# Optimization experiments

Measured on AMD Instinct MI355X. Metric: run time of the kernel, lower is better.

The kernel has to match this reference:

```python
import jax, jax.numpy as jnp
import numpy as np

EPS = 1e-5
N_LAYER = 2            # Mamba2 blocks per direction
D_STATE = 16
HEADDIM = 32
D_INNER = 256          # expand * d_model
NHEADS = D_INNER // HEADDIM
CONV_DIM = D_INNER + 2 * D_STATE
D_CONV = 4


def rmsnorm(x, w):
    return x * jax.lax.rsqrt(jnp.mean(x * x, axis=-1, keepdims=True) + EPS) * w


def causal_dwconv(x, w, b):
    # x: [B, L, C]; w: [C, K]; depthwise causal conv along L (torch conv1d groups=C, pad K-1, slice :L)
    out = jax.lax.conv_general_dilated(
        x.transpose(0, 2, 1), w[:, None, :], (1,), [(w.shape[1] - 1, 0)],
        dimension_numbers=('NCH', 'OIH', 'NCH'), feature_group_count=w.shape[0])
    return (out + b[:, None]).transpose(0, 2, 1)


def ssm_scan(dA, dtx, Bm, Cm):
    # dA:[B,L,H]  dtx:[B,L,H,P]  Bm,Cm:[B,L,N]  ->  y:[B,L,H,P]
    Bsz, L, H, P = dtx.shape
    N = Bm.shape[-1]
    h0 = jnp.zeros((Bsz, H, P, N), dtx.dtype)

    def step(h, ins):
        dA_t, dtx_t, B_t, C_t = ins
        h = h * dA_t[:, :, None, None] + jnp.einsum('bhp,bn->bhpn', dtx_t, B_t)
        return h, jnp.einsum('bhpn,bn->bhp', h, C_t)

    _, ys = jax.lax.scan(step, h0, (dA.transpose(1, 0, 2), dtx.transpose(1, 0, 2, 3),
                                    Bm.transpose(1, 0, 2), Cm.transpose(1, 0, 2)))
    return ys.transpose(1, 0, 2, 3)


def mamba2_block(h, in_w, cw, cb, dtb, a_log, d_skip, nw, ow):
    Bsz, L, _ = h.shape
    zxbcdt = jnp.einsum('bld,ed->ble', h, in_w)  # [B,L, 2*d_inner + 2*N + H]
    z = zxbcdt[..., :D_INNER]
    xBC = zxbcdt[..., D_INNER:D_INNER + CONV_DIM]
    dt = jax.nn.softplus(zxbcdt[..., D_INNER + CONV_DIM:] + dtb)  # [B,L,H]
    xBC = jax.nn.silu(causal_dwconv(xBC, cw, cb))
    xs = xBC[..., :D_INNER].reshape(Bsz, L, NHEADS, HEADDIM)
    Bm = xBC[..., D_INNER:D_INNER + D_STATE]
    Cm = xBC[..., D_INNER + D_STATE:]
    dA = jnp.exp(dt * (-jnp.exp(a_log)))                           # [B,L,H]
    y = ssm_scan(dA, dt[..., None] * xs, Bm, Cm) + d_skip[None, None, :, None] * xs
    y = rmsnorm(y.reshape(Bsz, L, D_INNER) * jax.nn.silu(z), nw)   # gated RMSNorm
    return jnp.einsum('ble,de->bld', y, ow)


def reference(x, buffer, fc_in_w, fc_in_b, blk_norm_w, in_proj_w, conv_w, conv_b,
              dt_bias, A_log, D, mixer_norm_w, out_proj_w, norm_f_w,
              fc_out_w, fc_out_b, out_lin_w, out_lin_b):
    n_state_buffer = buffer.shape[2]
    buf = jnp.concatenate([buffer, x[:, :, None]], axis=2)[:, :, -n_state_buffer:]
    h = jnp.einsum('bcl,dc->bld', buf, fc_in_w) + fc_in_b  # [B,L,d_model]

    def run_dir(hh, dir_idx):
        for l in range(N_LAYER):
            i = dir_idx * N_LAYER + l
            hh = hh + mamba2_block(rmsnorm(hh, blk_norm_w[i]), in_proj_w[i],
                                   conv_w[i], conv_b[i], dt_bias[i], A_log[i],
                                   D[i], mixer_norm_w[i], out_proj_w[i])
        return rmsnorm(hh, norm_f_w[dir_idx])

    hs = run_dir(h, 0) + jnp.flip(run_dir(jnp.flip(h, 1), 1), 1)
    y = jnp.einsum('bld,od->blo', hs, fc_out_w) + fc_out_b        # [B,L,cout]
    y = jnp.einsum('blo,kl->bok', y, out_lin_w)[..., 0] + out_lin_b[0]  # [B,cout]
    return y, buf


def setup_inputs():
    key = jax.random.key(0)
    ks = jax.random.split(key, 10)
    B, CIN, COUT, L, DM, NB = 1024, 96, 12, 32, 128, 4
    f = jnp.float32
    return {
        'x': jax.random.normal(ks[0], (B, CIN), f),
        'buffer': jax.random.normal(ks[1], (B, CIN, L), f),
        'fc_in_w': jax.random.normal(ks[2], (DM, CIN), f) * 0.05,
        'fc_in_b': jnp.zeros((DM,), f),
        'blk_norm_w': jnp.ones((NB, DM), f),
        'in_proj_w': jax.random.normal(ks[3], (NB, 2 * D_INNER + 2 * D_STATE + NHEADS, DM), f) * 0.05,
        'conv_w': jax.random.normal(ks[4], (NB, CONV_DIM, D_CONV), f) * 0.2,
        'conv_b': jnp.zeros((NB, CONV_DIM), f),
        'dt_bias': jax.random.normal(ks[5], (NB, NHEADS), f) * 0.1,
        'A_log': jnp.log(jax.random.uniform(ks[6], (NB, NHEADS), f, 1.0, 16.0)),
        'D': jnp.ones((NB, NHEADS), f),
        'mixer_norm_w': jnp.ones((NB, D_INNER), f),
        'out_proj_w': jax.random.normal(ks[7], (NB, DM, D_INNER), f) * 0.05,
        'norm_f_w': jnp.ones((2, DM), f),
        'fc_out_w': jax.random.normal(ks[8], (COUT, DM), f) * 0.05,
        'fc_out_b': jnp.zeros((COUT,), f),
        'out_lin_w': jax.random.normal(ks[9], (1, L), f) * 0.1,
        'out_lin_b': jnp.zeros((1,), f),
    }
```

## Files before the change

kernel.cpp:

```cpp
#include <hip/hip_runtime.h>
#include <hip/hip_bf16.h>
#include <math.h>

#define B_SZ   1024
#define CIN    96
#define COUT   12
#define LSEQ   32
#define DM     128
#define D_IN   256
#define D_ST   16
#define NH     8
#define HD     32
#define CONVD  288
#define EPROJ  552
#define EPSV   1e-5f

#define THREADS 512

typedef unsigned short ushort_t;
typedef unsigned int uint_t;
typedef __attribute__((ext_vector_type(8))) short short8;
typedef __attribute__((ext_vector_type(4))) float f32x4;

#define NIP (4*35*4*512)
#define NOP (4*8*8*512)
#define NFC (8*3*512)
__device__ ushort_t g_wip[NIP];
__device__ ushort_t g_wop[NOP];
__device__ ushort_t g_wfc[NFC];

__device__ __forceinline__ uint_t cvt2bf(float lo, float hi) {
    uint_t r;
    asm("v_cvt_pk_bf16_f32 %0, %1, %2" : "=v"(r) : "v"(lo), "v"(hi));
    return r;
}
__device__ __forceinline__ ushort_t f2bf(float f) {
    return (ushort_t)cvt2bf(f, f);
}
__device__ __forceinline__ float bf2f(ushort_t u) {
    return __uint_as_float((uint_t)u << 16);
}
__device__ __forceinline__ float siluf(float v) { return v / (1.f + __expf(-v)); }
__device__ __forceinline__ float softplusf_(float v) {
    return (v > 20.f) ? v : log1pf(__expf(v));
}

__device__ __forceinline__ ushort_t f2bf_sw(float f) {
    uint_t u = __float_as_uint(f);
    u += 0x7FFFu + ((u >> 16) & 1u);
    return (ushort_t)(u >> 16);
}

__global__ void prep_weights(const float* __restrict__ in_proj_w,
                             const float* __restrict__ out_proj_w,
                             const float* __restrict__ fc_in_w) {
    int idx = blockIdx.x * 256 + threadIdx.x;
    if (idx < NIP) {
        int f = idx >> 9, r = idx & 511;
        int l = r >> 3, j = r & 7;
        int li = f / 140, rem = f - li * 140;
        int nt = rem >> 2, kc = rem & 3;
        int e = nt * 16 + (l & 15);
        int d = kc * 32 + ((l >> 4) << 3) + j;
        float v = (e < EPROJ) ? in_proj_w[((size_t)li * EPROJ + e) * DM + d] : 0.f;
        g_wip[idx] = f2bf_sw(v);
    } else if (idx < NIP + NOP) {
        int i2 = idx - NIP;
        int f = i2 >> 9, r = i2 & 511;
        int l = r >> 3, j = r & 7;
        int li = f >> 6, rem = f & 63;
        int nt = rem >> 3, kc = rem & 7;
        int d = nt * 16 + (l & 15);
        int e = kc * 32 + ((l >> 4) << 3) + j;
        g_wop[i2] = f2bf_sw(out_proj_w[((size_t)li * DM + d) * D_IN + e]);
    } else if (idx < NIP + NOP + NFC) {
        int i2 = idx - NIP - NOP;
        int f = i2 >> 9, r = i2 & 511;
        int l = r >> 3, j = r & 7;
        int nt = f / 3, kc = f - nt * 3;
        int d = nt * 16 + (l & 15);
        int c = kc * 32 + ((l >> 4) << 3) + j;
        g_wfc[i2] = f2bf_sw(fc_in_w[d * CIN + c]);
    }
}

__global__ void init_out(const float* __restrict__ fc_out_b,
                         const float* __restrict__ out_lin_w,
                         const float* __restrict__ out_lin_b,
                         float* __restrict__ out_y) {
    int i = blockIdx.x * 256 + threadIdx.x;
    if (i >= B_SZ * COUT) return;
    int o = i % COUT;
    float s = 0.f;
#pragma unroll
    for (int t = 0; t < LSEQ; ++t) s += out_lin_w[t];
    out_y[i] = fc_out_b[o] * s + out_lin_b[0];
}

#define OFF_HH   0
#define OFF_BUFB 4224
#define OFF_HNB  6272
#define OFF_ZYB  8320
#define OFF_XB   12416
#define OFF_BCF  16512
#define OFF_DTA  17664
#define SMEM_WORDS 18176
#define SMEM_BYTES (SMEM_WORDS * 4)

__global__ __launch_bounds__(THREADS, 4)
void mamba_fused(const float* __restrict__ x,
                 const float* __restrict__ buffer,
                 const float* __restrict__ fc_in_b,
                 const float* __restrict__ blk_norm_w,
                 const float* __restrict__ conv_w,
                 const float* __restrict__ conv_b,
                 const float* __restrict__ dt_bias,
                 const float* __restrict__ A_log,
                 const float* __restrict__ D_skip,
                 const float* __restrict__ mixer_norm_w,
                 const float* __restrict__ norm_f_w,
                 const float* __restrict__ fc_out_w,
                 const float* __restrict__ out_lin_w,
                 float* __restrict__ out_y,
                 float* __restrict__ out_buf)
{
    const int b   = blockIdx.x >> 1;
    const int dir = blockIdx.x & 1;
    const int tid = threadIdx.x;

    extern __shared__ float sm[];
    float*    s_hh  = sm + OFF_HH;
    ushort_t* s_bufb= (ushort_t*)(sm + OFF_BUFB);
    ushort_t* s_hnb = (ushort_t*)(sm + OFF_HNB);
    ushort_t* s_zyb = (ushort_t*)(sm + OFF_ZYB);
    ushort_t* s_xb  = (ushort_t*)(sm + OFF_XB);
    float*    s_bcf = sm + OFF_BCF;
    float*    s_dtA = sm + OFF_DTA;

    const int wid  = tid >> 6;
    const int lane = tid & 63;
    const int quad = lane >> 4;

    {
        const float* bufp = buffer + (size_t)b * (CIN * LSEQ);
        const float* xp   = x + (size_t)b * CIN;
        float* obp        = out_buf + (size_t)b * (CIN * LSEQ);
        for (int i = tid; i < CIN * LSEQ; i += THREADS) {
            int c = i >> 5, l2 = i & 31;
            float v = (l2 < 31) ? bufp[i + 1] : xp[c];
            if (dir == 0) obp[i] = v;
            s_bufb[(l2 * 128 + c) ^ ((l2 & 7) << 3)] = f2bf(v);
        }
    }
    __syncthreads();

    {
        int mt = wid >> 2, row = mt * 16 + (lane & 15);
        const short8* ab = (const short8*)s_bufb;
        const ushort_t* wb = g_wfc + lane * 8;
#pragma unroll
        for (int pass = 0; pass < 2; ++pass) {
            int nt = (wid & 3) + pass * 4;
            f32x4 acc = {0.f, 0.f, 0.f, 0.f};
#pragma unroll
            for (int kc = 0; kc < 3; ++kc) {
                short8 av = ab[(row * 16 + kc * 4 + quad) ^ (row & 7)];
                short8 bv = *(const short8*)(wb + (nt * 3 + kc) * 512);
                acc = __builtin_amdgcn_mfma_f32_16x16x32_bf16(av, bv, acc, 0, 0, 0);
            }
            int d = nt * 16 + (lane & 15);
            float bias = fc_in_b[d];
#pragma unroll
            for (int r = 0; r < 4; ++r) {
                int t = mt * 16 + quad * 4 + r;
                int tt = dir ? (31 - t) : t;
                s_hh[tt * 132 + d] = acc[r] + bias;
            }
        }
    }
    __syncthreads();

    for (int lyr = 0; lyr < 2; ++lyr) {
        const int li = dir * 2 + lyr;

        {
            int t = tid >> 4, sl = tid & 15;
            const float* row = s_hh + t * 132;
            float v[8]; float ss = 0.f;
#pragma unroll
            for (int j = 0; j < 8; ++j) { v[j] = row[sl * 8 + j]; ss += v[j] * v[j]; }
            ss += __shfl_xor(ss, 1); ss += __shfl_xor(ss, 2);
            ss += __shfl_xor(ss, 4); ss += __shfl_xor(ss, 8);
            float scale = rsqrtf(ss * (1.f / DM) + EPSV);
            const float* nw = blk_norm_w + li * DM;
            uint_t w[4];
#pragma unroll
            for (int p = 0; p < 4; ++p) {
                int d0 = sl * 8 + p * 2;
                w[p] = cvt2bf(v[p * 2] * scale * nw[d0],
                              v[p * 2 + 1] * scale * nw[d0 + 1]);
            }
            uint4 q = make_uint4(w[0], w[1], w[2], w[3]);
            ((uint4*)s_hnb)[(t * 16 + sl) ^ (t & 7)] = q;
        }
        __syncthreads();

        {
            int mt = wid >> 2, row = mt * 16 + (lane & 15);
            const short8* ab = (const short8*)s_hnb;
            short8 a[4];
#pragma unroll
            for (int kc = 0; kc < 4; ++kc)
                a[kc] = ab[(row * 16 + kc * 4 + quad) ^ (row & 7)];

            const ushort_t* wbase = g_wip + (size_t)li * (35 * 4 * 512) + lane * 8;
            for (int nt = wid & 3; nt < 35; nt += 4) {
                f32x4 acc = {0.f, 0.f, 0.f, 0.f};
#pragma unroll
                for (int kc = 0; kc < 4; ++kc) {
                    short8 bv = *(const short8*)(wbase + (nt * 4 + kc) * 512);
                    acc = __builtin_amdgcn_mfma_f32_16x16x32_bf16(a[kc], bv, acc, 0, 0, 0);
                }
                int e = nt * 16 + (lane & 15);
#pragma unroll
                for (int r = 0; r < 4; ++r) {
                    int t = mt * 16 + quad * 4 + r;
                    float v = acc[r];
                    if (e < D_IN) {
                        s_zyb[(t * 256 + e) ^ ((t & 7) << 3)] = f2bf(siluf(v));
                    } else if (e < 512) {
                        s_xb[t * 256 + (e - D_IN)] = f2bf(v);
                    } else if (e < 544) {
                        s_bcf[t * 36 + (e - 512)] = v;
                    } else if (e < EPROJ) {
                        int hd2 = e - 544;
                        float dtv = softplusf_(v + dt_bias[li * NH + hd2]);
                        float aneg = -__expf(A_log[li * NH + hd2]);
                        s_dtA[t * 16 + hd2 * 2]     = dtv;
                        s_dtA[t * 16 + hd2 * 2 + 1] = __expf(dtv * aneg);
                    }
                }
            }
        }
        __syncthreads();

        if (tid < CONVD) {
            const int c = tid;
            const float4 wv = *(const float4*)(conv_w + ((size_t)li * CONVD + c) * 4);
            const float bias = conv_b[li * CONVD + c];
            float w0 = 0.f, w1 = 0.f, w2 = 0.f;
            if (c < D_IN) {
#pragma unroll
                for (int t = 0; t < 32; ++t) {
                    float cur = bf2f(s_xb[t * 256 + c]);
                    float acc = bias + w0 * wv.x + w1 * wv.y + w2 * wv.z + cur * wv.w;
                    s_xb[t * 256 + c] = f2bf(siluf(acc));
                    w0 = w1; w1 = w2; w2 = cur;
                }
            } else {
                const int ch = c - D_IN;
#pragma unroll
                for (int t = 0; t < 32; ++t) {
                    float cur = s_bcf[t * 36 + ch];
                    float acc = bias + w0 * wv.x + w1 * wv.y + w2 * wv.z + cur * wv.w;
                    s_bcf[t * 36 + ch] = siluf(acc);
                    w0 = w1; w1 = w2; w2 = cur;
                }
            }
        }
        __syncthreads();

        if (tid < 256) {
            int hd = tid >> 5, p = tid & 31;
            float dsk = D_skip[li * NH + hd];
            float st[16];
#pragma unroll
            for (int n = 0; n < 16; ++n) st[n] = 0.f;
#pragma unroll
            for (int t = 0; t < 32; ++t) {
                const float2 da = *(const float2*)(s_dtA + t * 16 + hd * 2);
                float dtv = da.x, dAv = da.y;
                float xsv = bf2f(s_xb[t * 256 + hd * HD + p]);
                float dtx = dtv * xsv;
                const f32x4* Bp = (const f32x4*)(s_bcf + t * 36);
                const f32x4* Cp = (const f32x4*)(s_bcf + t * 36 + 16);
                float acc0 = 0.f, acc1 = 0.f, acc2 = 0.f, acc3 = 0.f;
#pragma unroll
                for (int q = 0; q < 4; ++q) {
                    f32x4 Bv = Bp[q], Cv = Cp[q];
                    float* s4 = st + q * 4;
                    s4[0] = s4[0] * dAv + dtx * Bv.x;  acc0 += s4[0] * Cv.x;
                    s4[1] = s4[1] * dAv + dtx * Bv.y;  acc1 += s4[1] * Cv.y;
                    s4[2] = s4[2] * dAv + dtx * Bv.z;  acc2 += s4[2] * Cv.z;
                    s4[3] = s4[3] * dAv + dtx * Bv.w;  acc3 += s4[3] * Cv.w;
                }
                float y = (acc0 + acc1) + (acc2 + acc3) + dsk * xsv;
                s_xb[t * 256 + hd * HD + p] = f2bf(y);
            }
        }
        __syncthreads();

        {
            int t = tid >> 4, sl = tid & 15;
            float g[16]; float ss = 0.f;
#pragma unroll
            for (int j = 0; j < 16; ++j) {
                int e = j * 16 + sl;
                float yv = bf2f(s_xb[t * 256 + e]);
                float zv = bf2f(s_zyb[(t * 256 + e) ^ ((t & 7) << 3)]);
                float gv = yv * zv;
                g[j] = gv; ss += gv * gv;
            }
            ss += __shfl_xor(ss, 1); ss += __shfl_xor(ss, 2);
            ss += __shfl_xor(ss, 4); ss += __shfl_xor(ss, 8);
            float scale = rsqrtf(ss * (1.f / D_IN) + EPSV);
            const float* mw = mixer_norm_w + li * D_IN;
#pragma unroll
            for (int j = 0; j < 16; ++j) {
                int e = j * 16 + sl;
                s_zyb[(t * 256 + e) ^ ((t & 7) << 3)] = f2bf(g[j] * scale * mw[e]);
            }
        }
        __syncthreads();

        {
            int mt = wid >> 2, row = mt * 16 + (lane & 15);
            const short8* yb = (const short8*)s_zyb;
            const ushort_t* wb = g_wop + (size_t)li * (8 * 8 * 512) + lane * 8;
#pragma unroll
            for (int pass = 0; pass < 2; ++pass) {
                int nt = (wid & 3) + pass * 4;
                f32x4 acc = {0.f, 0.f, 0.f, 0.f};
#pragma unroll
                for (int kh = 0; kh < 2; ++kh) {
                    short8 a4[4];
#pragma unroll
                    for (int j = 0; j < 4; ++j)
                        a4[j] = yb[(row * 32 + (kh * 4 + j) * 4 + quad) ^ (row & 7)];
#pragma unroll
                    for (int j = 0; j < 4; ++j) {
                        short8 bv = *(const short8*)(wb + (nt * 8 + kh * 4 + j) * 512);
                        acc = __builtin_amdgcn_mfma_f32_16x16x32_bf16(a4[j], bv, acc, 0, 0, 0);
                    }
                }
                int d = nt * 16 + (lane & 15);
#pragma unroll
                for (int r = 0; r < 4; ++r)
                    s_hh[(mt * 16 + quad * 4 + r) * 132 + d] += acc[r];
            }
        }
        __syncthreads();
    }

    {
        int t = tid >> 4, sl = tid & 15;
        float* row = s_hh + t * 132;
        float v[8]; float ss = 0.f;
#pragma unroll
        for (int j = 0; j < 8; ++j) { v[j] = row[sl * 8 + j]; ss += v[j] * v[j]; }
        ss += __shfl_xor(ss, 1); ss += __shfl_xor(ss, 2);
        ss += __shfl_xor(ss, 4); ss += __shfl_xor(ss, 8);
        float scale = rsqrtf(ss * (1.f / DM) + EPSV);
        const float* nw = norm_f_w + dir * DM;
#pragma unroll
        for (int j = 0; j < 8; ++j) {
            int d = sl * 8 + j;
            row[d] = v[j] * scale * nw[d];
        }
    }
    __syncthreads();

    if (tid < COUT * LSEQ) {
        int o = tid >> 5, t = tid & 31;
        int t_out = dir ? (31 - t) : t;
        const float* wrow = fc_out_w + o * DM;
        const float* hrow = s_hh + t * 132;
        float acc = 0.f;
#pragma unroll
        for (int d = 0; d < DM; d += 4) {
            float4 wv = *(const float4*)(wrow + d);
            float4 hv = *(const float4*)(hrow + d);
            acc += hv.x * wv.x + hv.y * wv.y + hv.z * wv.z + hv.w * wv.w;
        }
        float part = acc * out_lin_w[t_out];
        part += __shfl_xor(part, 1);  part += __shfl_xor(part, 2);
        part += __shfl_xor(part, 4);  part += __shfl_xor(part, 8);
        part += __shfl_xor(part, 16);
        if (t == 0) atomicAdd(&out_y[b * COUT + o], part);
    }
}

extern "C" void kernel_launch(void* const* d_in, const int* in_sizes, int n_in,
                              void* d_out, int out_size, void* d_ws, size_t ws_size,
                              hipStream_t stream) {
    const float* x            = (const float*)d_in[0];
    const float* buffer      = (const float*)d_in[1];
    const float* fc_in_w     = (const float*)d_in[2];
    const float* fc_in_b     = (const float*)d_in[3];
    const float* blk_norm_w  = (const float*)d_in[4];
    const float* in_proj_w   = (const float*)d_in[5];
    const float* conv_w      = (const float*)d_in[6];
    const float* conv_b      = (const float*)d_in[7];
    const float* dt_bias     = (const float*)d_in[8];
    const float* A_log       = (const float*)d_in[9];
    const float* D_skip      = (const float*)d_in[10];
    const float* mixer_norm_w= (const float*)d_in[11];
    const float* out_proj_w  = (const float*)d_in[12];
    const float* norm_f_w    = (const float*)d_in[13];
    const float* fc_out_w    = (const float*)d_in[14];
    const float* fc_out_b    = (const float*)d_in[15];
    const float* out_lin_w   = (const float*)d_in[16];
    const float* out_lin_b   = (const float*)d_in[17];

    float* out_y   = (float*)d_out;
    float* out_buf = out_y + (size_t)B_SZ * COUT;

    prep_weights<<<(NIP + NOP + NFC + 255) / 256, 256, 0, stream>>>(
        in_proj_w, out_proj_w, fc_in_w);

    init_out<<<(B_SZ * COUT + 255) / 256, 256, 0, stream>>>(
        fc_out_b, out_lin_w, out_lin_b, out_y);

    (void)hipFuncSetAttribute((const void*)mamba_fused,
                              hipFuncAttributeMaxDynamicSharedMemorySize,
                              SMEM_BYTES);

    mamba_fused<<<B_SZ * 2, THREADS, SMEM_BYTES, stream>>>(
        x, buffer, fc_in_b, blk_norm_w, conv_w, conv_b,
        dt_bias, A_log, D_skip, mixer_norm_w, norm_f_w,
        fc_out_w, out_lin_w, out_y, out_buf);
}
```

Before: 265.7 us.

## Replace sequential SSM scan with chunked SSD matmul form using MFMA

Replaces the per-thread sequential 32-step state recurrence with the quadratic SSD formulation. A wave-level prefix sum builds the cumulative log-decay, MFMA computes C·Bᵀ, a masked decay is applied, and a second MFMA multiplies the result by dt·x. All 8 waves now take part instead of only 256 threads, and the work maps onto matrix cores. The cost is that B, C and the decay matrix are rounded to bf16, which lowers accuracy. It also reuses the input buffer region as scratch space.

```diff
diff --git a/kernel.cpp b/kernel.cpp
--- a/kernel.cpp
+++ b/kernel.cpp
@@ -21,6 +21,7 @@
 typedef unsigned int uint_t;
 typedef __attribute__((ext_vector_type(8))) short short8;
 typedef __attribute__((ext_vector_type(4))) float f32x4;
+typedef __attribute__((ext_vector_type(16))) float f32x16;
 
 #define NIP (4*35*4*512)
 #define NOP (4*8*8*512)
@@ -104,7 +105,8 @@
 #define OFF_XB   12416
 #define OFF_BCF  16512
 #define OFF_DTA  17664
-#define SMEM_WORDS 18176
+#define OFF_BCB  18176
+#define SMEM_WORDS 18688
 #define SMEM_BYTES (SMEM_WORDS * 4)
 
 __global__ __launch_bounds__(THREADS, 4)
@@ -136,6 +138,7 @@
     ushort_t* s_xb  = (ushort_t*)(sm + OFF_XB);
     float*    s_bcf = sm + OFF_BCF;
     float*    s_dtA = sm + OFF_DTA;
+    ushort_t* s_bcb = (ushort_t*)(sm + OFF_BCB);
 
     const int wid  = tid >> 6;
     const int lane = tid & 63;
@@ -237,7 +240,7 @@
                         float dtv = softplusf_(v + dt_bias[li * NH + hd2]);
                         float aneg = -__expf(A_log[li * NH + hd2]);
                         s_dtA[t * 16 + hd2 * 2]     = dtv;
-                        s_dtA[t * 16 + hd2 * 2 + 1] = __expf(dtv * aneg);
+                        s_dtA[t * 16 + hd2 * 2 + 1] = dtv * aneg;
                     }
                 }
             }
@@ -263,39 +266,67 @@
                 for (int t = 0; t < 32; ++t) {
                     float cur = s_bcf[t * 36 + ch];
                     float acc = bias + w0 * wv.x + w1 * wv.y + w2 * wv.z + cur * wv.w;
-                    s_bcf[t * 36 + ch] = siluf(acc);
+                    s_bcb[t * 32 + ch] = f2bf(siluf(acc));
                     w0 = w1; w1 = w2; w2 = cur;
                 }
             }
         }
         __syncthreads();
 
-        if (tid < 256) {
-            int hd = tid >> 5, p = tid & 31;
-            float dsk = D_skip[li * NH + hd];
-            float st[16];
-#pragma unroll
-            for (int n = 0; n < 16; ++n) st[n] = 0.f;
-#pragma unroll
-            for (int t = 0; t < 32; ++t) {
-                const float2 da = *(const float2*)(s_dtA + t * 16 + hd * 2);
-                float dtv = da.x, dAv = da.y;
-                float xsv = bf2f(s_xb[t * 256 + hd * HD + p]);
-                float dtx = dtv * xsv;
-                const f32x4* Bp = (const f32x4*)(s_bcf + t * 36);
-                const f32x4* Cp = (const f32x4*)(s_bcf + t * 36 + 16);
-                float acc0 = 0.f, acc1 = 0.f, acc2 = 0.f, acc3 = 0.f;
-#pragma unroll
-                for (int q = 0; q < 4; ++q) {
-                    f32x4 Bv = Bp[q], Cv = Cp[q];
-                    float* s4 = st + q * 4;
-                    s4[0] = s4[0] * dAv + dtx * Bv.x;  acc0 += s4[0] * Cv.x;
-                    s4[1] = s4[1] * dAv + dtx * Bv.y;  acc1 += s4[1] * Cv.y;
-                    s4[2] = s4[2] * dAv + dtx * Bv.z;  acc2 += s4[2] * Cv.z;
-                    s4[3] = s4[3] * dAv + dtx * Bv.w;  acc3 += s4[3] * Cv.w;
-                }
-                float y = (acc0 + acc1) + (acc2 + acc3) + dsk * xsv;
-                s_xb[t * 256 + hd * HD + p] = f2bf(y);
+        {
+            const int h  = wid;
+            const int tl = lane & 31;
+            const int hw = lane >> 5;
+            ushort_t* p_buf = (ushort_t*)(sm + OFF_BUFB) + h * 1024;
+
+            float Sv = s_dtA[tl * 16 + h * 2 + 1];
+#pragma unroll
+            for (int k = 1; k < 32; k <<= 1) {
+                int src = lane - ((tl >= k) ? k : 0);
+                float v = __shfl(Sv, src);
+                if (tl >= k) Sv += v;
+            }
+
+            short8 cfrag = *(const short8*)(s_bcb + tl * 32 + 16 + hw * 8);
+            short8 bfrag = *(const short8*)(s_bcb + tl * 32 + hw * 8);
+            f32x16 p = {0.f,0.f,0.f,0.f,0.f,0.f,0.f,0.f,0.f,0.f,0.f,0.f,0.f,0.f,0.f,0.f};
+            p = __builtin_amdgcn_mfma_f32_32x32x16_bf16(cfrag, bfrag, p, 0, 0, 0);
+
+#pragma unroll
+            for (int r = 0; r < 16; ++r) {
+                const int Kr = (r & 3) + 8 * (r >> 2);
+                int row = Kr + 4 * hw;
+                float Srow = __int_as_float(
+                    __builtin_amdgcn_ds_bpermute(row * 4, __float_as_int(Sv)));
+                float dec = __expf(Srow - Sv);
+                float val = (row >= tl) ? p[r] * dec : 0.f;
+                p_buf[row * 32 + tl] = f2bf(val);
+            }
+            asm volatile("s_waitcnt lgkmcnt(0)" ::: "memory");
+            __builtin_amdgcn_sched_barrier(0);
+
+            f32x16 acc = {0.f,0.f,0.f,0.f,0.f,0.f,0.f,0.f,0.f,0.f,0.f,0.f,0.f,0.f,0.f,0.f};
+#pragma unroll
+            for (int kc = 0; kc < 2; ++kc) {
+                short8 af = *(const short8*)(p_buf + tl * 32 + kc * 16 + hw * 8);
+                union { uint_t u[4]; short8 v; } bu;
+#pragma unroll
+                for (int jj = 0; jj < 4; ++jj) {
+                    int s0 = kc * 16 + hw * 8 + jj * 2;
+                    float x0 = bf2f(s_xb[s0 * 256 + h * HD + tl]) * s_dtA[s0 * 16 + h * 2];
+                    float x1 = bf2f(s_xb[(s0 + 1) * 256 + h * HD + tl]) * s_dtA[(s0 + 1) * 16 + h * 2];
+                    bu.u[jj] = cvt2bf(x0, x1);
+                }
+                acc = __builtin_amdgcn_mfma_f32_32x32x16_bf16(af, bu.v, acc, 0, 0, 0);
+            }
+
+            float dsk = D_skip[li * NH + h];
+#pragma unroll
+            for (int r = 0; r < 16; ++r) {
+                const int Kr = (r & 3) + 8 * (r >> 2);
+                int idx = (Kr + 4 * hw) * 256 + h * HD + tl;
+                float y = acc[r] + dsk * bf2f(s_xb[idx]);
+                s_xb[idx] = f2bf(y);
             }
         }
         __syncthreads();
```

Result: slower. 370.7 us (+39.5%).

## Split SSM scan over two time halves with carry-state correction

Applied to the files above, without the earlier changes.

The sequential 32-step scan previously used only 256 of 512 threads. Now both thread halves each scan 16 timesteps from a zero state. The first half's final state is shared through shared memory, and the second half's outputs are corrected by adding the decayed carry state contracted with C. This halves the serial scan depth, at the cost of an extra barrier, a correction pass, and an extra bf16 round-trip on the second-half outputs.

```diff
diff --git a/kernel.cpp b/kernel.cpp
--- a/kernel.cpp
+++ b/kernel.cpp
@@ -136,6 +136,7 @@
     ushort_t* s_xb  = (ushort_t*)(sm + OFF_XB);
     float*    s_bcf = sm + OFF_BCF;
     float*    s_dtA = sm + OFF_DTA;
+    float*    s_st  = sm + OFF_BUFB;
 
     const int wid  = tid >> 6;
     const int lane = tid & 63;
@@ -270,14 +271,18 @@
         }
         __syncthreads();
 
-        if (tid < 256) {
-            int hd = tid >> 5, p = tid & 31;
+        {
+            const int hp   = tid & 255;
+            const int half = tid >> 8;
+            const int hd = hp >> 5, p = hp & 31;
+            const int t0 = half * 16;
             float dsk = D_skip[li * NH + hd];
             float st[16];
 #pragma unroll
             for (int n = 0; n < 16; ++n) st[n] = 0.f;
 #pragma unroll
-            for (int t = 0; t < 32; ++t) {
+            for (int t5 = 0; t5 < 16; ++t5) {
+                int t = t0 + t5;
                 const float2 da = *(const float2*)(s_dtA + t * 16 + hd * 2);
                 float dtv = da.x, dAv = da.y;
                 float xsv = bf2f(s_xb[t * 256 + hd * HD + p]);
@@ -296,6 +301,37 @@
                 }
                 float y = (acc0 + acc1) + (acc2 + acc3) + dsk * xsv;
                 s_xb[t * 256 + hd * HD + p] = f2bf(y);
+            }
+            if (half == 0) {
+#pragma unroll
+                for (int n = 0; n < 16; ++n) s_st[n * 256 + hp] = st[n];
+            }
+            __syncthreads();
+
+            float h1[16];
+#pragma unroll
+            for (int n = 0; n < 16; ++n) h1[n] = s_st[n * 256 + hp];
+            float decprod = 1.f;
+            if (half) {
+#pragma unroll
+                for (int t = 16; t < 24; ++t) decprod *= s_dtA[t * 16 + hd * 2 + 1];
+            }
+            const int tf0 = 16 + half * 8;
+#pragma unroll
+            for (int t5 = 0; t5 < 8; ++t5) {
+                int t = tf0 + t5;
+                decprod *= s_dtA[t * 16 + hd * 2 + 1];
+                const float* Cp = s_bcf + t * 36 + 16;
+                float d0 = 0.f, d1 = 0.f, d2 = 0.f, d3 = 0.f;
+#pragma unroll
+                for (int n = 0; n < 4; ++n) {
+                    d0 += h1[n]      * Cp[n];
+                    d1 += h1[n + 4]  * Cp[n + 4];
+                    d2 += h1[n + 8]  * Cp[n + 8];
+                    d3 += h1[n + 12] * Cp[n + 12];
+                }
+                int idx = t * 256 + hd * HD + p;
+                s_xb[idx] = f2bf(bf2f(s_xb[idx]) + decprod * ((d0 + d1) + (d2 + d3)));
             }
         }
         __syncthreads();
```

New measurement: 366.3 us. +37.8%, slower.
